# Performance work log

Hardware: AMD Instinct MI355X
Metric: run time of the kernel (lower is better)

Reference implementation:

```python
import jax, jax.numpy as jnp
import numpy as np

D_K = 64
D_MODEL = 1024
N_HEADS = 16


def setup_inputs() -> dict:
    key = jax.random.key(0)
    ks = jax.random.split(key, 9)
    B, S = 2, 2048
    scale = 1.0 / np.sqrt(D_MODEL)
    inp = {
        "x": jax.random.normal(ks[0], (B, S, D_MODEL), dtype=jnp.float32),
        "w_q": jax.random.normal(ks[1], (D_MODEL, N_HEADS * D_K), dtype=jnp.float32) * scale,
        "b_q": jnp.zeros((N_HEADS * D_K,), dtype=jnp.float32),
        "w_k": jax.random.normal(ks[2], (D_MODEL, N_HEADS * D_K), dtype=jnp.float32) * scale,
        "b_k": jnp.zeros((N_HEADS * D_K,), dtype=jnp.float32),
        "w_v": jax.random.normal(ks[3], (D_MODEL, N_HEADS * D_K), dtype=jnp.float32) * scale,
        "b_v": jnp.zeros((N_HEADS * D_K,), dtype=jnp.float32),
        "w_o": jax.random.normal(ks[4], (N_HEADS * D_K, D_MODEL), dtype=jnp.float32) * scale,
        "b_o": jnp.zeros((D_MODEL,), dtype=jnp.float32),
    }
    return inp


def reference(x, w_q, b_q, w_k, b_k, w_v, b_v, w_o, b_o):
    B, S, _ = x.shape
    H, Dk = N_HEADS, D_K

    def split_heads(m):  # [B,S,H*Dk] -> [B,H,S,Dk]
        return m.reshape(B, S, H, Dk).transpose(0, 2, 1, 3)

    Q = split_heads(x @ w_q + b_q)
    K = split_heads(x @ w_k + b_k)
    V = split_heads(x @ w_v + b_v)

    scores = jnp.einsum("bhsd,bhtd->bhst", Q, K) / jnp.sqrt(jnp.float32(Dk))
    probs = jax.nn.softmax(scores, axis=-1)
    attn = jnp.einsum("bhst,bhtd->bhsd", probs, V)  # [B,H,S,Dk]
    attn = attn.transpose(0, 2, 1, 3).reshape(B, S, H * Dk)
    return attn @ w_o + b_o
```

## Files before the change

kernel.cpp:

```cpp
#include <hip/hip_runtime.h>
#include <math.h>

#define D_MODELc 1024
#define N_HEADSc 16
#define D_Kc     64
#define B_SZc    2
#define S_LENc   2048
#define NTOKc    (B_SZc * S_LENc)

using half8  = __attribute__((ext_vector_type(8))) _Float16;
using half4  = __attribute__((ext_vector_type(4))) _Float16;
using fp16x2 = __attribute__((ext_vector_type(2))) __fp16;
using float4v = __attribute__((ext_vector_type(4))) float;

__global__ __launch_bounds__(256) void cvt_all(
    const float* __restrict__ x,
    const float* __restrict__ W0, const float* __restrict__ W1,
    const float* __restrict__ W2, const float* __restrict__ W3,
    _Float16* __restrict__ wout, _Float16* __restrict__ xout)
{
    __shared__ float T[32][33];
    const int z = blockIdx.z;
    const int t = threadIdx.x;

    if (z == 4) {
        const int bid = blockIdx.y * 32 + blockIdx.x;
        #pragma unroll
        for (int c = 0; c < 2; ++c) {
            const int i = bid * 512 + c * 256 + t;
            float4v a = ((const float4v*)x)[2 * i];
            float4v b = ((const float4v*)x)[2 * i + 1];
            half8 h;
            h[0] = (_Float16)a[0]; h[1] = (_Float16)a[1];
            h[2] = (_Float16)a[2]; h[3] = (_Float16)a[3];
            h[4] = (_Float16)b[0]; h[5] = (_Float16)b[1];
            h[6] = (_Float16)b[2]; h[7] = (_Float16)b[3];
            ((half8*)xout)[i] = h;
        }
        return;
    }

    const float* W = (z == 0) ? W0 : (z == 1) ? W1 : (z == 2) ? W2 : W3;
    _Float16* O = wout + (size_t)z * 1024 * 1024;

    const int k0 = blockIdx.x * 32;
    const int n0 = blockIdx.y * 32;
    {
        const int r = t >> 3, c4 = (t & 7) * 4;
        float4v v = *(const float4v*)(W + (size_t)(k0 + r) * 1024 + n0 + c4);
        T[r][c4 + 0] = v[0]; T[r][c4 + 1] = v[1];
        T[r][c4 + 2] = v[2]; T[r][c4 + 3] = v[3];
    }
    __syncthreads();
    {
        const int rn = t >> 3, ck4 = (t & 7) * 4;
        half4 h;
        h[0] = (_Float16)T[ck4 + 0][rn];
        h[1] = (_Float16)T[ck4 + 1][rn];
        h[2] = (_Float16)T[ck4 + 2][rn];
        h[3] = (_Float16)T[ck4 + 3][rn];
        *(half4*)(O + (size_t)(n0 + rn) * 1024 + k0 + ck4) = h;
    }
}

__global__ __launch_bounds__(256) void gemm_qkv(
    const _Float16* __restrict__ A, const _Float16* __restrict__ BtAll,
    const float* __restrict__ bias0, const float* __restrict__ bias1,
    const float* __restrict__ bias2, _Float16* __restrict__ Cout)
{
    __shared__ _Float16 Als[2][128 * 32];
    __shared__ _Float16 Bls[2][128 * 32];

    constexpr int K = 1024;
    const int tid = threadIdx.x;
    const int m0  = blockIdx.x * 128;
    const int n0  = blockIdx.y * 128;
    const int z   = blockIdx.z;

    const _Float16* Bt  = BtAll + (size_t)z * 1024 * 1024;
    const float* bias   = (z == 0) ? bias0 : (z == 1) ? bias1 : bias2;
    const float qscale  = (z == 0) ? 0.18033688011112042f : 1.0f;

    const int wave = tid >> 6, lane = tid & 63;
    const int wr = wave >> 1, wc = wave & 1;
    const int quad = lane >> 4, l16 = lane & 15;

    float4v acc[4][4];
    #pragma unroll
    for (int i = 0; i < 4; ++i)
        #pragma unroll
        for (int j = 0; j < 4; ++j)
            acc[i][j] = (float4v){0.f, 0.f, 0.f, 0.f};

    for (int k0 = 0; k0 < K; k0 += 64) {
        #pragma unroll
        for (int c = 0; c < 2; ++c) {
            const int i   = c * 256 + tid;
            const int row = i >> 2, kc = i & 3;
            #pragma unroll
            for (int h = 0; h < 2; ++h) {
                __builtin_amdgcn_global_load_lds(
                    (const __attribute__((address_space(1))) void*)
                        (A + (size_t)(m0 + row) * K + k0 + h * 32 + kc * 8),
                    (__attribute__((address_space(3))) void*)(Als[h] + i * 8),
                    16, 0, 0);
                __builtin_amdgcn_global_load_lds(
                    (const __attribute__((address_space(1))) void*)
                        (Bt + (size_t)(n0 + row) * K + k0 + h * 32 + kc * 8),
                    (__attribute__((address_space(3))) void*)(Bls[h] + i * 8),
                    16, 0, 0);
            }
        }
        __syncthreads();

        half8 af[4][2], bf[4][2];
        #pragma unroll
        for (int i = 0; i < 4; ++i) {
            const int r = (wr * 64 + i * 16 + l16) * 32 + quad * 8;
            af[i][0] = *(const half8*)(Als[0] + r);
            af[i][1] = *(const half8*)(Als[1] + r);
        }
        #pragma unroll
        for (int j = 0; j < 4; ++j) {
            const int r = (wc * 64 + j * 16 + l16) * 32 + quad * 8;
            bf[j][0] = *(const half8*)(Bls[0] + r);
            bf[j][1] = *(const half8*)(Bls[1] + r);
        }
        #pragma unroll
        for (int i = 0; i < 4; ++i)
            #pragma unroll
            for (int j = 0; j < 4; ++j) {
                acc[i][j] = __builtin_amdgcn_mfma_f32_16x16x32_f16(
                    af[i][0], bf[j][0], acc[i][j], 0, 0, 0);
                acc[i][j] = __builtin_amdgcn_mfma_f32_16x16x32_f16(
                    af[i][1], bf[j][1], acc[i][j], 0, 0, 0);
            }
        __syncthreads();
    }

    if (z != 2) {
        #pragma unroll
        for (int i = 0; i < 4; ++i) {
            const int rbase = m0 + wr * 64 + i * 16 + quad * 4;
            #pragma unroll
            for (int j = 0; j < 4; ++j) {
                const int col = n0 + wc * 64 + j * 16 + l16;
                const float bv = bias[col];
                #pragma unroll
                for (int r = 0; r < 4; ++r) {
                    const float v = (acc[i][j][r] + bv) * qscale;
                    const int n = rbase + r;
                    const int b = n >> 11, s = n & 2047;
                    const int h = col >> 6, d = col & 63;
                    _Float16* C = Cout + (size_t)z * NTOKc * D_MODELc;
                    C[(((size_t)(b * N_HEADSc + h)) * S_LENc + s) * D_Kc + d] =
                        (_Float16)v;
                }
            }
        }
    } else {
        #pragma unroll
        for (int i = 0; i < 4; ++i) {
            const int rbase = m0 + wr * 64 + i * 16 + quad * 4;
            const int b = rbase >> 11, s0 = rbase & 2047;
            #pragma unroll
            for (int j = 0; j < 4; ++j) {
                const int col = n0 + wc * 64 + j * 16 + l16;
                const float bv = bias[col];
                const int h = col >> 6, d = col & 63;
                half4 hv;
                #pragma unroll
                for (int r = 0; r < 4; ++r)
                    hv[r] = (_Float16)(acc[i][j][r] + bv);
                _Float16* C = Cout + (size_t)2 * NTOKc * D_MODELc;
                *(half4*)(C + (((size_t)(b * N_HEADSc + h)) * D_Kc + d) *
                          S_LENc + s0) = hv;
            }
        }
    }
}

__global__ __launch_bounds__(256) void gemm_out(
    const _Float16* __restrict__ A, const _Float16* __restrict__ Bt,
    const float* __restrict__ bias, float* __restrict__ C)
{
    __shared__ _Float16 Als[2][64 * 32];
    __shared__ _Float16 Bls[2][128 * 32];

    constexpr int K = 1024;
    const int tid = threadIdx.x;
    const int m0  = blockIdx.x * 64;
    const int n0  = blockIdx.y * 128;

    const int wave = tid >> 6, lane = tid & 63;
    const int wr = wave >> 1, wc = wave & 1;
    const int quad = lane >> 4, l16 = lane & 15;

    float4v acc[2][4];
    #pragma unroll
    for (int i = 0; i < 2; ++i)
        #pragma unroll
        for (int j = 0; j < 4; ++j)
            acc[i][j] = (float4v){0.f, 0.f, 0.f, 0.f};

    for (int k0 = 0; k0 < K; k0 += 64) {
        {
            const int row = tid >> 2, kc = tid & 3;
            #pragma unroll
            for (int h = 0; h < 2; ++h)
                __builtin_amdgcn_global_load_lds(
                    (const __attribute__((address_space(1))) void*)
                        (A + (size_t)(m0 + row) * K + k0 + h * 32 + kc * 8),
                    (__attribute__((address_space(3))) void*)(Als[h] + tid * 8),
                    16, 0, 0);
        }
        #pragma unroll
        for (int c = 0; c < 2; ++c) {
            const int i = c * 256 + tid;
            const int row = i >> 2, kc = i & 3;
            #pragma unroll
            for (int h = 0; h < 2; ++h)
                __builtin_amdgcn_global_load_lds(
                    (const __attribute__((address_space(1))) void*)
                        (Bt + (size_t)(n0 + row) * K + k0 + h * 32 + kc * 8),
                    (__attribute__((address_space(3))) void*)(Bls[h] + i * 8),
                    16, 0, 0);
        }
        __syncthreads();

        half8 af[2][2], bf[4][2];
        #pragma unroll
        for (int i = 0; i < 2; ++i) {
            const int r = (wr * 32 + i * 16 + l16) * 32 + quad * 8;
            af[i][0] = *(const half8*)(Als[0] + r);
            af[i][1] = *(const half8*)(Als[1] + r);
        }
        #pragma unroll
        for (int j = 0; j < 4; ++j) {
            const int r = (wc * 64 + j * 16 + l16) * 32 + quad * 8;
            bf[j][0] = *(const half8*)(Bls[0] + r);
            bf[j][1] = *(const half8*)(Bls[1] + r);
        }
        #pragma unroll
        for (int i = 0; i < 2; ++i)
            #pragma unroll
            for (int j = 0; j < 4; ++j) {
                acc[i][j] = __builtin_amdgcn_mfma_f32_16x16x32_f16(
                    af[i][0], bf[j][0], acc[i][j], 0, 0, 0);
                acc[i][j] = __builtin_amdgcn_mfma_f32_16x16x32_f16(
                    af[i][1], bf[j][1], acc[i][j], 0, 0, 0);
            }
        __syncthreads();
    }

    #pragma unroll
    for (int i = 0; i < 2; ++i) {
        const int rbase = m0 + wr * 32 + i * 16 + quad * 4;
        #pragma unroll
        for (int j = 0; j < 4; ++j) {
            const int col = n0 + wc * 64 + j * 16 + l16;
            const float bv = bias[col];
            #pragma unroll
            for (int r = 0; r < 4; ++r)
                C[(size_t)(rbase + r) * 1024 + col] = acc[i][j][r] + bv;
        }
    }
}

__global__ __launch_bounds__(256) void attn_mfma(
    const _Float16* __restrict__ Qb, const _Float16* __restrict__ Kb,
    const _Float16* __restrict__ Vtg, _Float16* __restrict__ Op,
    float* __restrict__ Lp)
{
    __shared__ _Float16 Ks[64 * 64];
    __shared__ _Float16 Vt[64 * 64];
    __shared__ _Float16 Ps[128 * 64];

    const int tid  = threadIdx.x;
    const int wv   = tid >> 6;
    const int lane = tid & 63;
    const int quad = lane >> 4;
    const int l16  = lane & 15;
    const int sw   = (l16 & 7) << 3;

    const int q0 = blockIdx.x * 128;
    const int bh = blockIdx.y;
    const int sp = blockIdx.z;
    const int kb = sp * (S_LENc / 2);
    const int kend = kb + S_LENc / 2;

    const _Float16* Qsl = Qb  + (size_t)bh * S_LENc * D_Kc;
    const _Float16* Ksl = Kb  + (size_t)bh * S_LENc * D_Kc;
    const _Float16* Vsl = Vtg + (size_t)bh * S_LENc * D_Kc;

    half8 aq[2][2];
    #pragma unroll
    for (int qf = 0; qf < 2; ++qf) {
        const int row = q0 + wv * 32 + qf * 16 + l16;
        aq[qf][0] = *(const half8*)(Qsl + (size_t)row * 64 + quad * 8);
        aq[qf][1] = *(const half8*)(Qsl + (size_t)row * 64 + 32 + quad * 8);
    }

    float4v O[2][4];
    #pragma unroll
    for (int qf = 0; qf < 2; ++qf)
        #pragma unroll
        for (int nt = 0; nt < 4; ++nt)
            O[qf][nt] = (float4v){0.f, 0.f, 0.f, 0.f};
    float lr[2] = {0.f, 0.f};

    const int sr  = tid >> 2;
    const int sg  = (tid & 3) * 16;
    const int swS = (sr & 7) << 3;
    const int wA  = (sr * 64 + sg) ^ swS;
    const int wB  = (sr * 64 + sg + 8) ^ swS;

    half8 k0 = *(const half8*)(Ksl + (size_t)(kb + sr) * 64 + sg);
    half8 k1 = *(const half8*)(Ksl + (size_t)(kb + sr) * 64 + sg + 8);
    half8 v0 = *(const half8*)(Vsl + (size_t)sr * S_LENc + kb + sg);
    half8 v1 = *(const half8*)(Vsl + (size_t)sr * S_LENc + kb + sg + 8);

    for (int t0 = kb; t0 < kend; t0 += 64) {
        __syncthreads();
        *(half8*)(Ks + wA) = k0;
        *(half8*)(Ks + wB) = k1;
        *(half8*)(Vt + wA) = v0;
        *(half8*)(Vt + wB) = v1;
        __syncthreads();

        const int tn = t0 + 64;
        if (tn < kend) {
            k0 = *(const half8*)(Ksl + (size_t)(tn + sr) * 64 + sg);
            k1 = *(const half8*)(Ksl + (size_t)(tn + sr) * 64 + sg + 8);
            v0 = *(const half8*)(Vsl + (size_t)sr * S_LENc + tn + sg);
            v1 = *(const half8*)(Vsl + (size_t)sr * S_LENc + tn + sg + 8);
        }

        half8 kf[4][2];
        #pragma unroll
        for (int nt = 0; nt < 4; ++nt) {
            const int base = (nt * 16 + l16) * 64;
            kf[nt][0] = *(const half8*)(Ks + ((base + quad * 8) ^ sw));
            kf[nt][1] = *(const half8*)(Ks + ((base + 32 + quad * 8) ^ sw));
        }

        #pragma unroll
        for (int qf = 0; qf < 2; ++qf) {
            float4v st[4];
            __builtin_amdgcn_s_setprio(1);
            #pragma unroll
            for (int nt = 0; nt < 4; ++nt) {
                st[nt] = __builtin_amdgcn_mfma_f32_16x16x32_f16(
                    kf[nt][0], aq[qf][0], (float4v){0.f, 0.f, 0.f, 0.f}, 0, 0, 0);
                st[nt] = __builtin_amdgcn_mfma_f32_16x16x32_f16(
                    kf[nt][1], aq[qf][1], st[nt], 0, 0, 0);
            }
            __builtin_amdgcn_s_setprio(0);
            float ls = 0.f;
            const int rowP = (wv * 32 + qf * 16 + l16) * 64;
            #pragma unroll
            for (int nt = 0; nt < 4; ++nt) {
                const float p0 = __builtin_amdgcn_exp2f(fminf(st[nt][0], 15.5f));
                const float p1 = __builtin_amdgcn_exp2f(fminf(st[nt][1], 15.5f));
                const float p2 = __builtin_amdgcn_exp2f(fminf(st[nt][2], 15.5f));
                const float p3 = __builtin_amdgcn_exp2f(fminf(st[nt][3], 15.5f));
                ls += (p0 + p1) + (p2 + p3);
                union { fp16x2 h2[2]; half4 h4; } u;
                u.h2[0] = __builtin_amdgcn_cvt_pkrtz(p0, p1);
                u.h2[1] = __builtin_amdgcn_cvt_pkrtz(p2, p3);
                *(half4*)(Ps + ((rowP + nt * 16 + quad * 4) ^ sw)) = u.h4;
            }
            lr[qf] += ls;
        }

        half8 bvv[4][2];
        #pragma unroll
        for (int nt = 0; nt < 4; ++nt) {
            const int base = (nt * 16 + l16) * 64;
            bvv[nt][0] = *(const half8*)(Vt + ((base + quad * 8) ^ sw));
            bvv[nt][1] = *(const half8*)(Vt + ((base + 32 + quad * 8) ^ sw));
        }
        #pragma unroll
        for (int qf = 0; qf < 2; ++qf) {
            const int rowP = (wv * 32 + qf * 16 + l16) * 64;
            half8 ap0 = *(const half8*)(Ps + ((rowP + quad * 8) ^ sw));
            half8 ap1 = *(const half8*)(Ps + ((rowP + 32 + quad * 8) ^ sw));
            __builtin_amdgcn_s_setprio(1);
            #pragma unroll
            for (int nt = 0; nt < 4; ++nt) {
                O[qf][nt] = __builtin_amdgcn_mfma_f32_16x16x32_f16(
                    ap0, bvv[nt][0], O[qf][nt], 0, 0, 0);
                O[qf][nt] = __builtin_amdgcn_mfma_f32_16x16x32_f16(
                    ap1, bvv[nt][1], O[qf][nt], 0, 0, 0);
            }
            __builtin_amdgcn_s_setprio(0);
        }
    }

    const size_t qgb = (size_t)bh * S_LENc;
    #pragma unroll
    for (int qf = 0; qf < 2; ++qf) {
        float t = lr[qf];
        t += __shfl_xor(t, 16, 64);
        t += __shfl_xor(t, 32, 64);
        if (quad == 0)
            Lp[(size_t)sp * 65536 + qgb + q0 + wv * 32 + qf * 16 + l16] = t;
        #pragma unroll
        for (int r = 0; r < 4; ++r) {
            const int q = q0 + wv * 32 + qf * 16 + quad * 4 + r;
            _Float16* dst = Op + ((size_t)sp * 65536 + qgb + q) * 64;
            #pragma unroll
            for (int nt = 0; nt < 4; ++nt)
                dst[nt * 16 + l16] = (_Float16)O[qf][nt][r];
        }
    }
}

__global__ __launch_bounds__(256) void attn_combine(
    const _Float16* __restrict__ Op, const float* __restrict__ Lp,
    _Float16* __restrict__ Ab)
{
    const int i  = blockIdx.x * 256 + threadIdx.x;
    const int e0 = i * 8;
    const int qg = e0 >> 6;
    const int d0 = e0 & 63;
    const int bh = qg >> 11, q = qg & 2047;
    const int b  = bh >> 4,  h = bh & 15;

    const float inv = 1.0f / (Lp[qg] + Lp[65536 + qg]);
    half8 o0 = *(const half8*)(Op + (size_t)qg * 64 + d0);
    half8 o1 = *(const half8*)(Op + ((size_t)65536 + qg) * 64 + d0);
    half8 hv;
    #pragma unroll
    for (int j = 0; j < 8; ++j)
        hv[j] = (_Float16)(((float)o0[j] + (float)o1[j]) * inv);
    *(half8*)(Ab + ((size_t)(b * S_LENc + q)) * 1024 + h * 64 + d0) = hv;
}

extern "C" void kernel_launch(void* const* d_in, const int* in_sizes, int n_in,
                              void* d_out, int out_size, void* d_ws, size_t ws_size,
                              hipStream_t stream)
{
    const float* x  = (const float*)d_in[0];
    const float* wq = (const float*)d_in[1];
    const float* bq = (const float*)d_in[2];
    const float* wk = (const float*)d_in[3];
    const float* bk = (const float*)d_in[4];
    const float* wv = (const float*)d_in[5];
    const float* bv = (const float*)d_in[6];
    const float* wo = (const float*)d_in[7];
    const float* bo = (const float*)d_in[8];
    float* out = (float*)d_out;

    const size_t M1 = 1024 * 1024;
    const size_t M4 = 4 * M1;
    _Float16* xh = (_Float16*)d_ws;
    _Float16* wh = xh + M4;
    _Float16* Qh = wh + M4;
    _Float16* Oph = Qh + 3 * M4;
    float*    Lp  = (float*)(Oph + 2 * M4);
    _Float16* Ah = xh;

    cvt_all<<<dim3(32, 32, 5), dim3(256), 0, stream>>>(
        x, wq, wk, wv, wo, wh, xh);
    gemm_qkv<<<dim3(NTOKc / 128, D_MODELc / 128, 3), dim3(256), 0, stream>>>(
        xh, wh, bq, bk, bv, Qh);
    attn_mfma<<<dim3(S_LENc / 128, B_SZc * N_HEADSc, 2), dim3(256), 0, stream>>>(
        Qh, Qh + M4, Qh + 2 * M4, Oph, Lp);
    attn_combine<<<dim3(NTOKc * D_MODELc / 8 / 256), dim3(256), 0, stream>>>(
        Oph, Lp, Ah);
    gemm_out<<<dim3(NTOKc / 64, D_MODELc / 128), dim3(256), 0, stream>>>(
        Ah, wh + 3 * M1, bo, out);
}
```

Baseline: 208.2 us.

## Split attention key range into four parts when workspace allows, drop register prefetch

The attention kernel now takes a runtime key-split length, and the host picks four key splits instead of two when the workspace is large enough. The combine kernel loops over a variable number of partial outputs and row sums. The register double-buffered prefetch of the next K/V tile is removed, so global loads now happen inside the loop just before the shared-memory store. More splits give more blocks to fill the GPU, at the cost of more partial-output traffic and a longer combine step. Losing the prefetch exposes load latency in each iteration.

```diff
diff --git a/kernel.cpp b/kernel.cpp
--- a/kernel.cpp
+++ b/kernel.cpp
@@ -270,7 +270,7 @@
 __global__ __launch_bounds__(256) void attn_mfma(
     const _Float16* __restrict__ Qb, const _Float16* __restrict__ Kb,
     const _Float16* __restrict__ Vtg, _Float16* __restrict__ Op,
-    float* __restrict__ Lp)
+    float* __restrict__ Lp, int SL)
 {
     __shared__ _Float16 Ks[64 * 64];
     __shared__ _Float16 Vt[64 * 64];
@@ -286,8 +286,8 @@
     const int q0 = blockIdx.x * 128;
     const int bh = blockIdx.y;
     const int sp = blockIdx.z;
-    const int kb = sp * (S_LENc / 2);
-    const int kend = kb + S_LENc / 2;
+    const int kb = sp * SL;
+    const int kend = kb + SL;
 
     const _Float16* Qsl = Qb  + (size_t)bh * S_LENc * D_Kc;
     const _Float16* Ksl = Kb  + (size_t)bh * S_LENc * D_Kc;
@@ -315,26 +315,17 @@
     const int wA  = (sr * 64 + sg) ^ swS;
     const int wB  = (sr * 64 + sg + 8) ^ swS;
 
-    half8 k0 = *(const half8*)(Ksl + (size_t)(kb + sr) * 64 + sg);
-    half8 k1 = *(const half8*)(Ksl + (size_t)(kb + sr) * 64 + sg + 8);
-    half8 v0 = *(const half8*)(Vsl + (size_t)sr * S_LENc + kb + sg);
-    half8 v1 = *(const half8*)(Vsl + (size_t)sr * S_LENc + kb + sg + 8);
-
     for (int t0 = kb; t0 < kend; t0 += 64) {
+        half8 k0 = *(const half8*)(Ksl + (size_t)(t0 + sr) * 64 + sg);
+        half8 k1 = *(const half8*)(Ksl + (size_t)(t0 + sr) * 64 + sg + 8);
+        half8 v0 = *(const half8*)(Vsl + (size_t)sr * S_LENc + t0 + sg);
+        half8 v1 = *(const half8*)(Vsl + (size_t)sr * S_LENc + t0 + sg + 8);
         __syncthreads();
         *(half8*)(Ks + wA) = k0;
         *(half8*)(Ks + wB) = k1;
         *(half8*)(Vt + wA) = v0;
         *(half8*)(Vt + wB) = v1;
         __syncthreads();
-
-        const int tn = t0 + 64;
-        if (tn < kend) {
-            k0 = *(const half8*)(Ksl + (size_t)(tn + sr) * 64 + sg);
-            k1 = *(const half8*)(Ksl + (size_t)(tn + sr) * 64 + sg + 8);
-            v0 = *(const half8*)(Vsl + (size_t)sr * S_LENc + tn + sg);
-            v1 = *(const half8*)(Vsl + (size_t)sr * S_LENc + tn + sg + 8);
-        }
 
         half8 kf[4][2];
         #pragma unroll
@@ -418,7 +409,7 @@
 
 __global__ __launch_bounds__(256) void attn_combine(
     const _Float16* __restrict__ Op, const float* __restrict__ Lp,
-    _Float16* __restrict__ Ab)
+    _Float16* __restrict__ Ab, int SP)
 {
     const int i  = blockIdx.x * 256 + threadIdx.x;
     const int e0 = i * 8;
@@ -427,13 +418,22 @@
     const int bh = qg >> 11, q = qg & 2047;
     const int b  = bh >> 4,  h = bh & 15;
 
-    const float inv = 1.0f / (Lp[qg] + Lp[65536 + qg]);
-    half8 o0 = *(const half8*)(Op + (size_t)qg * 64 + d0);
-    half8 o1 = *(const half8*)(Op + ((size_t)65536 + qg) * 64 + d0);
+    float l = 0.f;
+    for (int j = 0; j < SP; ++j)
+        l += Lp[(size_t)j * 65536 + qg];
+    const float inv = 1.0f / l;
+
+    float o[8] = {0.f, 0.f, 0.f, 0.f, 0.f, 0.f, 0.f, 0.f};
+    for (int j = 0; j < SP; ++j) {
+        half8 ov = *(const half8*)(Op + ((size_t)j * 65536 + qg) * 64 + d0);
+        #pragma unroll
+        for (int k = 0; k < 8; ++k)
+            o[k] += (float)ov[k];
+    }
     half8 hv;
     #pragma unroll
-    for (int j = 0; j < 8; ++j)
-        hv[j] = (_Float16)(((float)o0[j] + (float)o1[j]) * inv);
+    for (int k = 0; k < 8; ++k)
+        hv[k] = (_Float16)(o[k] * inv);
     *(half8*)(Ab + ((size_t)(b * S_LENc + q)) * 1024 + h * 64 + d0) = hv;
 }
 
@@ -454,21 +454,25 @@
 
     const size_t M1 = 1024 * 1024;
     const size_t M4 = 4 * M1;
+
+    const size_t need4 = 2 * M4 * 9 + 4 * 4 * 65536;
+    const int SP = (ws_size >= need4) ? 4 : 2;
+
     _Float16* xh = (_Float16*)d_ws;
     _Float16* wh = xh + M4;
     _Float16* Qh = wh + M4;
     _Float16* Oph = Qh + 3 * M4;
-    float*    Lp  = (float*)(Oph + 2 * M4);
+    float*    Lp  = (float*)(Oph + (size_t)SP * M4);
     _Float16* Ah = xh;
 
     cvt_all<<<dim3(32, 32, 5), dim3(256), 0, stream>>>(
         x, wq, wk, wv, wo, wh, xh);
     gemm_qkv<<<dim3(NTOKc / 128, D_MODELc / 128, 3), dim3(256), 0, stream>>>(
         xh, wh, bq, bk, bv, Qh);
-    attn_mfma<<<dim3(S_LENc / 128, B_SZc * N_HEADSc, 2), dim3(256), 0, stream>>>(
-        Qh, Qh + M4, Qh + 2 * M4, Oph, Lp);
+    attn_mfma<<<dim3(S_LENc / 128, B_SZc * N_HEADSc, SP), dim3(256), 0, stream>>>(
+        Qh, Qh + M4, Qh + 2 * M4, Oph, Lp, S_LENc / SP);
     attn_combine<<<dim3(NTOKc * D_MODELc / 8 / 256), dim3(256), 0, stream>>>(
-        Oph, Lp, Ah);
+        Oph, Lp, Ah, SP);
     gemm_out<<<dim3(NTOKc / 64, D_MODELc / 128), dim3(256), 0, stream>>>(
         Ah, wh + 3 * M1, bo, out);
 }
```

Measured after the change: 213.9 us. 1.03x slower.

## Stage K/V tiles via direct global-to-LDS loads with double-buffered K

Applied to the files above, without the earlier changes.

The attention kernel no longer stages K and V through registers with ds_write. It issues global_load_lds DMA copies straight into shared memory, and double-buffers the K tile so the next tile is prefetched during the PV phase. To fit the fixed lane-to-LDS mapping of the DMA path, the XOR swizzle is replaced by a per-row rotation, applied to the global source column and to all LDS reads, including the P buffer. V stays single-buffered and is loaded at the top of each iteration, so its latency is only hidden behind the QK and softmax work. Correctness relies on the compiler inserting the vmcnt waits before the barriers.

```diff
diff --git a/kernel.cpp b/kernel.cpp
--- a/kernel.cpp
+++ b/kernel.cpp
@@ -272,7 +272,7 @@
     const _Float16* __restrict__ Vtg, _Float16* __restrict__ Op,
     float* __restrict__ Lp)
 {
-    __shared__ _Float16 Ks[64 * 64];
+    __shared__ _Float16 Ks[2][64 * 64];
     __shared__ _Float16 Vt[64 * 64];
     __shared__ _Float16 Ps[128 * 64];
 
@@ -281,7 +281,9 @@
     const int lane = tid & 63;
     const int quad = lane >> 4;
     const int l16  = lane & 15;
-    const int sw   = (l16 & 7) << 3;
+    const int rotl = (l16 & 7) << 3;
+    const int cA   = (quad * 8 + rotl) & 63;
+    const int cB   = (quad * 8 + 32 + rotl) & 63;
 
     const int q0 = blockIdx.x * 128;
     const int bh = blockIdx.y;
@@ -293,6 +295,34 @@
     const _Float16* Ksl = Kb  + (size_t)bh * S_LENc * D_Kc;
     const _Float16* Vsl = Vtg + (size_t)bh * S_LENc * D_Kc;
 
+    const int sR = tid >> 3;
+    const int sC = (((tid & 7) - ((tid >> 3) & 7)) & 7) << 3;
+    const _Float16* gK = Ksl + (size_t)sR * 64 + sC;
+    const _Float16* gV = Vsl + (size_t)sR * S_LENc + sC;
+
+#define STAGE_KT(BUF, T0)                                                    \
+    {                                                                        \
+        _Pragma("unroll")                                                    \
+        for (int c = 0; c < 2; ++c)                                          \
+            __builtin_amdgcn_global_load_lds(                                \
+                (const __attribute__((address_space(1))) void*)              \
+                    (gK + (size_t)(T0) * 64 + c * 2048),                     \
+                (__attribute__((address_space(3))) void*)                    \
+                    (Ks[BUF] + tid * 8 + c * 2048),                          \
+                16, 0, 0);                                                   \
+    }
+#define STAGE_VT(T0)                                                         \
+    {                                                                        \
+        _Pragma("unroll")                                                    \
+        for (int c = 0; c < 2; ++c)                                          \
+            __builtin_amdgcn_global_load_lds(                                \
+                (const __attribute__((address_space(1))) void*)              \
+                    (gV + (T0) + c * 32 * S_LENc),                           \
+                (__attribute__((address_space(3))) void*)                    \
+                    (Vt + tid * 8 + c * 2048),                               \
+                16, 0, 0);                                                   \
+    }
+
     half8 aq[2][2];
     #pragma unroll
     for (int qf = 0; qf < 2; ++qf) {
@@ -309,39 +339,22 @@
             O[qf][nt] = (float4v){0.f, 0.f, 0.f, 0.f};
     float lr[2] = {0.f, 0.f};
 
-    const int sr  = tid >> 2;
-    const int sg  = (tid & 3) * 16;
-    const int swS = (sr & 7) << 3;
-    const int wA  = (sr * 64 + sg) ^ swS;
-    const int wB  = (sr * 64 + sg + 8) ^ swS;
-
-    half8 k0 = *(const half8*)(Ksl + (size_t)(kb + sr) * 64 + sg);
-    half8 k1 = *(const half8*)(Ksl + (size_t)(kb + sr) * 64 + sg + 8);
-    half8 v0 = *(const half8*)(Vsl + (size_t)sr * S_LENc + kb + sg);
-    half8 v1 = *(const half8*)(Vsl + (size_t)sr * S_LENc + kb + sg + 8);
-
+    STAGE_KT(0, kb);
+    STAGE_VT(kb);
+
+    int cur = 0;
     for (int t0 = kb; t0 < kend; t0 += 64) {
         __syncthreads();
-        *(half8*)(Ks + wA) = k0;
-        *(half8*)(Ks + wB) = k1;
-        *(half8*)(Vt + wA) = v0;
-        *(half8*)(Vt + wB) = v1;
-        __syncthreads();
-
-        const int tn = t0 + 64;
-        if (tn < kend) {
-            k0 = *(const half8*)(Ksl + (size_t)(tn + sr) * 64 + sg);
-            k1 = *(const half8*)(Ksl + (size_t)(tn + sr) * 64 + sg + 8);
-            v0 = *(const half8*)(Vsl + (size_t)sr * S_LENc + tn + sg);
-            v1 = *(const half8*)(Vsl + (size_t)sr * S_LENc + tn + sg + 8);
-        }
-
+        if (t0 != kb)
+            STAGE_VT(t0);
+
+        const _Float16* KsC = Ks[cur];
         half8 kf[4][2];
         #pragma unroll
         for (int nt = 0; nt < 4; ++nt) {
             const int base = (nt * 16 + l16) * 64;
-            kf[nt][0] = *(const half8*)(Ks + ((base + quad * 8) ^ sw));
-            kf[nt][1] = *(const half8*)(Ks + ((base + 32 + quad * 8) ^ sw));
+            kf[nt][0] = *(const half8*)(KsC + base + cA);
+            kf[nt][1] = *(const half8*)(KsC + base + cB);
         }
 
         #pragma unroll
@@ -368,23 +381,27 @@
                 union { fp16x2 h2[2]; half4 h4; } u;
                 u.h2[0] = __builtin_amdgcn_cvt_pkrtz(p0, p1);
                 u.h2[1] = __builtin_amdgcn_cvt_pkrtz(p2, p3);
-                *(half4*)(Ps + ((rowP + nt * 16 + quad * 4) ^ sw)) = u.h4;
+                *(half4*)(Ps + rowP + ((nt * 16 + quad * 4 + rotl) & 63)) = u.h4;
             }
             lr[qf] += ls;
         }
+
+        __syncthreads();
+        if (t0 + 64 < kend)
+            STAGE_KT(cur ^ 1, t0 + 64);
 
         half8 bvv[4][2];
         #pragma unroll
         for (int nt = 0; nt < 4; ++nt) {
             const int base = (nt * 16 + l16) * 64;
-            bvv[nt][0] = *(const half8*)(Vt + ((base + quad * 8) ^ sw));
-            bvv[nt][1] = *(const half8*)(Vt + ((base + 32 + quad * 8) ^ sw));
+            bvv[nt][0] = *(const half8*)(Vt + base + cA);
+            bvv[nt][1] = *(const half8*)(Vt + base + cB);
         }
         #pragma unroll
         for (int qf = 0; qf < 2; ++qf) {
             const int rowP = (wv * 32 + qf * 16 + l16) * 64;
-            half8 ap0 = *(const half8*)(Ps + ((rowP + quad * 8) ^ sw));
-            half8 ap1 = *(const half8*)(Ps + ((rowP + 32 + quad * 8) ^ sw));
+            half8 ap0 = *(const half8*)(Ps + rowP + cA);
+            half8 ap1 = *(const half8*)(Ps + rowP + cB);
             __builtin_amdgcn_s_setprio(1);
             #pragma unroll
             for (int nt = 0; nt < 4; ++nt) {
@@ -395,7 +412,10 @@
             }
             __builtin_amdgcn_s_setprio(0);
         }
-    }
+        cur ^= 1;
+    }
+#undef STAGE_KT
+#undef STAGE_VT
 
     const size_t qgb = (size_t)bh * S_LENc;
     #pragma unroll
```

New measurement: 205.4 us. Within noise of the previous version (-1.3%).
